# Optimization experiments

Measured on AMD Instinct MI355X. Metric: run time of the kernel, lower is better.

The kernel has to match this reference:

```python
import jax, jax.numpy as jnp
import numpy as np

NBINS = 256

def _rescale_0_1(img):
    return (img + 1.0) * (127.0 / 255.0)

def _rescale_back(img):
    return img * (255.0 / 127.0) - 1.0

def _rgb_to_yuv_y(img):
    # tf.image.rgb_to_yuv luma coefficients; only Y channel is used downstream
    return img[..., 0] * 0.299 + img[..., 1] * 0.587 + img[..., 2] * 0.114

def _equalize_histogram(image):
    # tf.histogram_fixed_width over [0,1] with 256 bins (values clipped to range)
    idx = jnp.clip((image * NBINS).astype(jnp.int32), 0, NBINS - 1)
    hist = jnp.zeros((NBINS,), jnp.int32).at[idx.reshape(-1)].add(1)
    cdf = jnp.cumsum(hist)
    cdf_min = jnp.min(cdf)
    pix_cnt = image.shape[0] * image.shape[1]
    return (cdf - cdf_min).astype(jnp.float32) / jnp.float32(pix_cnt - 1)

def _interpolate(dx, dy, x):
    # brute-force searchsorted substitute: first index where dx - x > 0
    del_vals = dx[jnp.newaxis, :] - x[:, jnp.newaxis]          # [N, 256]
    ind_1 = jnp.argmax(jnp.sign(del_vals), axis=1)             # first positive
    ind_0 = jnp.clip(ind_1 - 1, 0, NBINS - 1)
    dx0, dx1 = dx[ind_0], dx[ind_1]
    dy0, dy1 = dy[ind_0], dy[ind_1]
    denom = dx1 - dx0
    safe_denom = jnp.where(denom == 0, jnp.float32(1.0), denom)
    interp = dy0 + (dy1 - dy0) * (x - dx0) / safe_denom
    return jnp.where(x <= dx[0], dy[0], jnp.where(x >= dx[-1], dy[-1], interp))

def setup_inputs() -> dict:
    key = jax.random.key(0)
    k1, k2 = jax.random.split(key)
    H, W = 1024, 1024
    src = jax.random.uniform(k1, (H, W, 3), jnp.float32, minval=-1.0, maxval=1.0)
    tgt = jax.random.uniform(k2, (H, W, 3), jnp.float32, minval=-1.0, maxval=1.0)
    return {"src": src, "tgt": tgt}

def reference(src, tgt):
    src = _rescale_0_1(src)
    tgt = _rescale_0_1(tgt)
    tgt_y = _rgb_to_yuv_y(tgt)
    h, w = src.shape[0], src.shape[1]
    floating_space = jnp.clip(jnp.arange(0.0, 1.00001, 1.0 / 255.0, dtype=jnp.float32), 0.0, 1.0)
    source = src[:, :, 0]
    cdfsrc = _equalize_histogram(source)
    cdftgt = _equalize_histogram(tgt_y)
    pxmap = _interpolate(cdftgt, floating_space, cdfsrc)
    pxmap = _interpolate(floating_space, pxmap, source.reshape(h * w))
    pxmap = pxmap.reshape(h, w, 1)
    res = jnp.clip(pxmap, 0.0, 1.0)
    return _rescale_back(res)
```

## Files before the change

kernel.cpp:

```cpp
#include <hip/hip_runtime.h>

#define NBINS 256

__device__ __forceinline__ float fs_val(int j) {
    const float c = (float)(1.0 / 255.0);
    float v = (float)j * c;
    return v > 1.0f ? 1.0f : v;
}

__device__ __forceinline__ int bin_of(float s) {
    int i = (int)(s * 256.0f);
    i = i < 0 ? 0 : i;
    i = i > NBINS - 1 ? NBINS - 1 : i;
    return i;
}

__global__ void hm_hist(const float* __restrict__ src,
                        const float* __restrict__ tgt,
                        int* __restrict__ histS, int* __restrict__ histT,
                        int nquad) {
    __shared__ int hs[NBINS];
    __shared__ int ht[NBINS];
    for (int i = threadIdx.x; i < NBINS; i += blockDim.x) { hs[i] = 0; ht[i] = 0; }
    __syncthreads();

    const float c1 = (float)(127.0 / 255.0);
    int tid = blockIdx.x * blockDim.x + threadIdx.x;
    int stride = gridDim.x * blockDim.x;

    for (int q = tid; q < nquad; q += stride) {
        const float4* s4 = (const float4*)(src + 12 * (size_t)q);
        float4 a = s4[0], b = s4[1], c = s4[2];
        float p0 = (a.x + 1.0f) * c1;
        float p1 = (a.w + 1.0f) * c1;
        float p2 = (b.z + 1.0f) * c1;
        float p3 = (c.y + 1.0f) * c1;
        atomicAdd(&hs[bin_of(p0)], 1);
        atomicAdd(&hs[bin_of(p1)], 1);
        atomicAdd(&hs[bin_of(p2)], 1);
        atomicAdd(&hs[bin_of(p3)], 1);

        const float4* t4 = (const float4*)(tgt + 12 * (size_t)q);
        float4 ta = t4[0], tb = t4[1], tc = t4[2];
        {
            float r = (ta.x + 1.0f) * c1, g = (ta.y + 1.0f) * c1, bb = (ta.z + 1.0f) * c1;
            float y = r * 0.299f + g * 0.587f + bb * 0.114f;
            atomicAdd(&ht[bin_of(y)], 1);
        }
        {
            float r = (ta.w + 1.0f) * c1, g = (tb.x + 1.0f) * c1, bb = (tb.y + 1.0f) * c1;
            float y = r * 0.299f + g * 0.587f + bb * 0.114f;
            atomicAdd(&ht[bin_of(y)], 1);
        }
        {
            float r = (tb.z + 1.0f) * c1, g = (tb.w + 1.0f) * c1, bb = (tc.x + 1.0f) * c1;
            float y = r * 0.299f + g * 0.587f + bb * 0.114f;
            atomicAdd(&ht[bin_of(y)], 1);
        }
        {
            float r = (tc.y + 1.0f) * c1, g = (tc.z + 1.0f) * c1, bb = (tc.w + 1.0f) * c1;
            float y = r * 0.299f + g * 0.587f + bb * 0.114f;
            atomicAdd(&ht[bin_of(y)], 1);
        }
    }
    __syncthreads();
    for (int i = threadIdx.x; i < NBINS; i += blockDim.x) {
        if (hs[i]) atomicAdd(&histS[i], hs[i]);
        if (ht[i]) atomicAdd(&histT[i], ht[i]);
    }
}

__global__ void hm_cdf_map(const int* __restrict__ histS,
                           const int* __restrict__ histT,
                           float* __restrict__ pxmap, int npix) {
    __shared__ int sS[NBINS];
    __shared__ int sT[NBINS];
    __shared__ float cdfT[NBINS];
    int t = threadIdx.x;
    sS[t] = histS[t];
    sT[t] = histT[t];
    __syncthreads();
    for (int off = 1; off < NBINS; off <<= 1) {
        int vS = sS[t], vT = sT[t];
        int aS = (t >= off) ? sS[t - off] : 0;
        int aT = (t >= off) ? sT[t - off] : 0;
        __syncthreads();
        sS[t] = vS + aS;
        sT[t] = vT + aT;
        __syncthreads();
    }
    int minS = sS[0], minT = sT[0];
    float denomN = (float)(npix - 1);
    float xS = (float)(sS[t] - minS) / denomN;
    cdfT[t] = (float)(sT[t] - minT) / denomN;
    __syncthreads();

    float res;
    if (xS <= cdfT[0]) {
        res = fs_val(0);
    } else if (xS >= cdfT[NBINS - 1]) {
        res = fs_val(NBINS - 1);
    } else {
        int lo = 0, hi = NBINS - 1;
        while (hi - lo > 1) {
            int mid = (lo + hi) >> 1;
            if (cdfT[mid] > xS) hi = mid; else lo = mid;
        }
        int j1 = hi, j0 = hi - 1;
        float dx0 = cdfT[j0], dx1 = cdfT[j1];
        float dy0 = fs_val(j0), dy1 = fs_val(j1);
        res = dy0 + (dy1 - dy0) * (xS - dx0) / (dx1 - dx0);
    }
    pxmap[t] = res;
}

__global__ void hm_apply(const float* __restrict__ src,
                         const float* __restrict__ pxmap,
                         float* __restrict__ out, int nquad) {
    __shared__ float pm[NBINS];
    for (int i = threadIdx.x; i < NBINS; i += blockDim.x) pm[i] = pxmap[i];
    __syncthreads();

    const float c1 = (float)(127.0 / 255.0);
    const float c2 = (float)(255.0 / 127.0);
    int tid = blockIdx.x * blockDim.x + threadIdx.x;
    int stride = gridDim.x * blockDim.x;

    for (int q = tid; q < nquad; q += stride) {
        const float4* s4 = (const float4*)(src + 12 * (size_t)q);
        float4 a = s4[0], b = s4[1], c = s4[2];
        float xs0 = a.x, xs1 = a.w, xs2 = b.z, xs3 = c.y;
        float4 o;
        float xv[4] = {xs0, xs1, xs2, xs3};
        float ov[4];
        #pragma unroll
        for (int k = 0; k < 4; ++k) {
            float x = (xv[k] + 1.0f) * c1;
            float r;
            if (x <= 0.0f) {
                r = pm[0];
            } else if (x >= 1.0f) {
                r = pm[NBINS - 1];
            } else {
                int g = (int)(x * 255.0f) + 1;
                g = g < 1 ? 1 : (g > NBINS - 1 ? NBINS - 1 : g);
                while (g < NBINS - 1 && fs_val(g) <= x) ++g;
                while (g > 1 && fs_val(g - 1) > x) --g;
                int j1 = g, j0 = g - 1;
                float dx0 = fs_val(j0), dx1 = fs_val(j1);
                r = pm[j0] + (pm[j1] - pm[j0]) * (x - dx0) / (dx1 - dx0);
            }
            r = r < 0.0f ? 0.0f : (r > 1.0f ? 1.0f : r);
            ov[k] = r * c2 - 1.0f;
        }
        o.x = ov[0]; o.y = ov[1]; o.z = ov[2]; o.w = ov[3];
        ((float4*)out)[q] = o;
    }
}

extern "C" void kernel_launch(void* const* d_in, const int* in_sizes, int n_in,
                              void* d_out, int out_size, void* d_ws, size_t ws_size,
                              hipStream_t stream) {
    const float* src = (const float*)d_in[0];
    const float* tgt = (const float*)d_in[1];
    float* out = (float*)d_out;

    int npix = out_size;
    int nquad = npix >> 2;

    int* histS = (int*)d_ws;
    int* histT = histS + NBINS;
    float* pxmap = (float*)(histT + NBINS);

    hipMemsetAsync(d_ws, 0, 2 * NBINS * sizeof(int), stream);

    hm_hist<<<256, 256, 0, stream>>>(src, tgt, histS, histT, nquad);

    hm_cdf_map<<<1, NBINS, 0, stream>>>(histS, histT, pxmap, npix);

    int blocks = (nquad + 255) / 256;
    hm_apply<<<blocks, 256, 0, stream>>>(src, pxmap, out, nquad);
}
```

Measured before the change: 83.35 us.

## Fuse histogram, CDF mapping and apply into one cooperative kernel

Replaces the memset and three kernel launches with a single cooperative kernel of 512 blocks that builds the histograms, grid-syncs, has every block redundantly compute the CDF and pixel map, and then writes the output. Each thread keeps the source values of its first two quads in registers so those pixels are not re-read. This removes launch gaps and the separate memset, at the cost of two grid-wide barriers and redundant per-block scan work. Zeroing the global histogram with atomicExch before the first grid sync depends on the sync ordering to be correct.

```diff
diff --git a/kernel.cpp b/kernel.cpp
--- a/kernel.cpp
+++ b/kernel.cpp
@@ -1,6 +1,9 @@
 #include <hip/hip_runtime.h>
+#include <hip/hip_cooperative_groups.h>
 
 #define NBINS 256
+
+namespace cg = cooperative_groups;
 
 __device__ __forceinline__ float fs_val(int j) {
     const float c = (float)(1.0 / 255.0);
@@ -15,84 +18,122 @@
     return i;
 }
 
-__global__ void hm_hist(const float* __restrict__ src,
-                        const float* __restrict__ tgt,
-                        int* __restrict__ histS, int* __restrict__ histT,
-                        int nquad) {
+__device__ __forceinline__ float4 hist_quad(const float* __restrict__ src,
+                                            const float* __restrict__ tgt,
+                                            int q, int* hs, int* ht) {
+    const float c1 = (float)(127.0 / 255.0);
+    const float4* s4 = (const float4*)(src + 12 * (size_t)q);
+    float4 a = s4[0], b = s4[1], c = s4[2];
+    float p0 = (a.x + 1.0f) * c1;
+    float p1 = (a.w + 1.0f) * c1;
+    float p2 = (b.z + 1.0f) * c1;
+    float p3 = (c.y + 1.0f) * c1;
+    atomicAdd(&hs[bin_of(p0)], 1);
+    atomicAdd(&hs[bin_of(p1)], 1);
+    atomicAdd(&hs[bin_of(p2)], 1);
+    atomicAdd(&hs[bin_of(p3)], 1);
+
+    const float4* t4 = (const float4*)(tgt + 12 * (size_t)q);
+    float4 ta = t4[0], tb = t4[1], tc = t4[2];
+    {
+        float r = (ta.x + 1.0f) * c1, g = (ta.y + 1.0f) * c1, bb = (ta.z + 1.0f) * c1;
+        float y = r * 0.299f + g * 0.587f + bb * 0.114f;
+        atomicAdd(&ht[bin_of(y)], 1);
+    }
+    {
+        float r = (ta.w + 1.0f) * c1, g = (tb.x + 1.0f) * c1, bb = (tb.y + 1.0f) * c1;
+        float y = r * 0.299f + g * 0.587f + bb * 0.114f;
+        atomicAdd(&ht[bin_of(y)], 1);
+    }
+    {
+        float r = (tb.z + 1.0f) * c1, g = (tb.w + 1.0f) * c1, bb = (tc.x + 1.0f) * c1;
+        float y = r * 0.299f + g * 0.587f + bb * 0.114f;
+        atomicAdd(&ht[bin_of(y)], 1);
+    }
+    {
+        float r = (tc.y + 1.0f) * c1, g = (tc.z + 1.0f) * c1, bb = (tc.w + 1.0f) * c1;
+        float y = r * 0.299f + g * 0.587f + bb * 0.114f;
+        atomicAdd(&ht[bin_of(y)], 1);
+    }
+    return make_float4(p0, p1, p2, p3);
+}
+
+__device__ __forceinline__ float map1(float x, const float* pm) {
+    const float c2 = (float)(255.0 / 127.0);
+    float r;
+    if (x <= 0.0f) {
+        r = pm[0];
+    } else if (x >= 1.0f) {
+        r = pm[NBINS - 1];
+    } else {
+        int g = (int)(x * 255.0f) + 1;
+        g = g < 1 ? 1 : (g > NBINS - 1 ? NBINS - 1 : g);
+        while (g < NBINS - 1 && fs_val(g) <= x) ++g;
+        while (g > 1 && fs_val(g - 1) > x) --g;
+        int j1 = g, j0 = g - 1;
+        float dx0 = fs_val(j0), dx1 = fs_val(j1);
+        r = pm[j0] + (pm[j1] - pm[j0]) * (x - dx0) / (dx1 - dx0);
+    }
+    r = r < 0.0f ? 0.0f : (r > 1.0f ? 1.0f : r);
+    return r * c2 - 1.0f;
+}
+
+__global__ void __launch_bounds__(256, 4)
+hm_fused(const float* __restrict__ src, const float* __restrict__ tgt,
+         float* __restrict__ out, int* __restrict__ histS, int* __restrict__ histT,
+         int nquad, int npix) {
     __shared__ int hs[NBINS];
     __shared__ int ht[NBINS];
-    for (int i = threadIdx.x; i < NBINS; i += blockDim.x) { hs[i] = 0; ht[i] = 0; }
+    __shared__ float cdfT[NBINS];
+    __shared__ float pm[NBINS];
+
+    cg::grid_group grid = cg::this_grid();
+
+    const int t = threadIdx.x;
+    const int gid = blockIdx.x * blockDim.x + t;
+    const int nthreads = gridDim.x * blockDim.x;
+
+    hs[t] = 0;
+    ht[t] = 0;
+    if (gid < NBINS)          atomicExch(&histS[gid], 0);
+    else if (gid < 2 * NBINS) atomicExch(&histT[gid - NBINS], 0);
     __syncthreads();
 
-    const float c1 = (float)(127.0 / 255.0);
-    int tid = blockIdx.x * blockDim.x + threadIdx.x;
-    int stride = gridDim.x * blockDim.x;
+    const int q0 = gid;
+    const int q1 = gid + nthreads;
+    float4 xa = make_float4(0.f, 0.f, 0.f, 0.f);
+    float4 xb = make_float4(0.f, 0.f, 0.f, 0.f);
+    if (q0 < nquad) xa = hist_quad(src, tgt, q0, hs, ht);
+    if (q1 < nquad) xb = hist_quad(src, tgt, q1, hs, ht);
+    for (int q = gid + 2 * nthreads; q < nquad; q += nthreads)
+        (void)hist_quad(src, tgt, q, hs, ht);
+    __syncthreads();
 
-    for (int q = tid; q < nquad; q += stride) {
-        const float4* s4 = (const float4*)(src + 12 * (size_t)q);
-        float4 a = s4[0], b = s4[1], c = s4[2];
-        float p0 = (a.x + 1.0f) * c1;
-        float p1 = (a.w + 1.0f) * c1;
-        float p2 = (b.z + 1.0f) * c1;
-        float p3 = (c.y + 1.0f) * c1;
-        atomicAdd(&hs[bin_of(p0)], 1);
-        atomicAdd(&hs[bin_of(p1)], 1);
-        atomicAdd(&hs[bin_of(p2)], 1);
-        atomicAdd(&hs[bin_of(p3)], 1);
+    grid.sync();
 
-        const float4* t4 = (const float4*)(tgt + 12 * (size_t)q);
-        float4 ta = t4[0], tb = t4[1], tc = t4[2];
-        {
-            float r = (ta.x + 1.0f) * c1, g = (ta.y + 1.0f) * c1, bb = (ta.z + 1.0f) * c1;
-            float y = r * 0.299f + g * 0.587f + bb * 0.114f;
-            atomicAdd(&ht[bin_of(y)], 1);
-        }
-        {
-            float r = (ta.w + 1.0f) * c1, g = (tb.x + 1.0f) * c1, bb = (tb.y + 1.0f) * c1;
-            float y = r * 0.299f + g * 0.587f + bb * 0.114f;
-            atomicAdd(&ht[bin_of(y)], 1);
-        }
-        {
-            float r = (tb.z + 1.0f) * c1, g = (tb.w + 1.0f) * c1, bb = (tc.x + 1.0f) * c1;
-            float y = r * 0.299f + g * 0.587f + bb * 0.114f;
-            atomicAdd(&ht[bin_of(y)], 1);
-        }
-        {
-            float r = (tc.y + 1.0f) * c1, g = (tc.z + 1.0f) * c1, bb = (tc.w + 1.0f) * c1;
-            float y = r * 0.299f + g * 0.587f + bb * 0.114f;
-            atomicAdd(&ht[bin_of(y)], 1);
-        }
-    }
-    __syncthreads();
-    for (int i = threadIdx.x; i < NBINS; i += blockDim.x) {
-        if (hs[i]) atomicAdd(&histS[i], hs[i]);
-        if (ht[i]) atomicAdd(&histT[i], ht[i]);
-    }
-}
+    if (hs[t]) atomicAdd(&histS[t], hs[t]);
+    if (ht[t]) atomicAdd(&histT[t], ht[t]);
 
-__global__ void hm_cdf_map(const int* __restrict__ histS,
-                           const int* __restrict__ histT,
-                           float* __restrict__ pxmap, int npix) {
-    __shared__ int sS[NBINS];
-    __shared__ int sT[NBINS];
-    __shared__ float cdfT[NBINS];
-    int t = threadIdx.x;
-    sS[t] = histS[t];
-    sT[t] = histT[t];
+    grid.sync();
+
+    int vS = histS[t];
+    int vT = histT[t];
+    hs[t] = vS;
+    ht[t] = vT;
     __syncthreads();
     for (int off = 1; off < NBINS; off <<= 1) {
-        int vS = sS[t], vT = sT[t];
-        int aS = (t >= off) ? sS[t - off] : 0;
-        int aT = (t >= off) ? sT[t - off] : 0;
+        int cS = hs[t], cT = ht[t];
+        int aS = (t >= off) ? hs[t - off] : 0;
+        int aT = (t >= off) ? ht[t - off] : 0;
         __syncthreads();
-        sS[t] = vS + aS;
-        sT[t] = vT + aT;
+        hs[t] = cS + aS;
+        ht[t] = cT + aT;
         __syncthreads();
     }
-    int minS = sS[0], minT = sT[0];
+    int minS = hs[0], minT = ht[0];
     float denomN = (float)(npix - 1);
-    float xS = (float)(sS[t] - minS) / denomN;
-    cdfT[t] = (float)(sT[t] - minT) / denomN;
+    float xS = (float)(hs[t] - minS) / denomN;
+    cdfT[t] = (float)(ht[t] - minT) / denomN;
     __syncthreads();
 
     float res;
@@ -111,49 +152,25 @@
         float dy0 = fs_val(j0), dy1 = fs_val(j1);
         res = dy0 + (dy1 - dy0) * (xS - dx0) / (dx1 - dx0);
     }
-    pxmap[t] = res;
-}
-
-__global__ void hm_apply(const float* __restrict__ src,
-                         const float* __restrict__ pxmap,
-                         float* __restrict__ out, int nquad) {
-    __shared__ float pm[NBINS];
-    for (int i = threadIdx.x; i < NBINS; i += blockDim.x) pm[i] = pxmap[i];
+    pm[t] = res;
     __syncthreads();
 
+    if (q0 < nquad) {
+        float4 o = make_float4(map1(xa.x, pm), map1(xa.y, pm), map1(xa.z, pm), map1(xa.w, pm));
+        ((float4*)out)[q0] = o;
+    }
+    if (q1 < nquad) {
+        float4 o = make_float4(map1(xb.x, pm), map1(xb.y, pm), map1(xb.z, pm), map1(xb.w, pm));
+        ((float4*)out)[q1] = o;
+    }
     const float c1 = (float)(127.0 / 255.0);
-    const float c2 = (float)(255.0 / 127.0);
-    int tid = blockIdx.x * blockDim.x + threadIdx.x;
-    int stride = gridDim.x * blockDim.x;
-
-    for (int q = tid; q < nquad; q += stride) {
+    for (int q = gid + 2 * nthreads; q < nquad; q += nthreads) {
         const float4* s4 = (const float4*)(src + 12 * (size_t)q);
         float4 a = s4[0], b = s4[1], c = s4[2];
-        float xs0 = a.x, xs1 = a.w, xs2 = b.z, xs3 = c.y;
-        float4 o;
-        float xv[4] = {xs0, xs1, xs2, xs3};
-        float ov[4];
-        #pragma unroll
-        for (int k = 0; k < 4; ++k) {
-            float x = (xv[k] + 1.0f) * c1;
-            float r;
-            if (x <= 0.0f) {
-                r = pm[0];
-            } else if (x >= 1.0f) {
-                r = pm[NBINS - 1];
-            } else {
-                int g = (int)(x * 255.0f) + 1;
-                g = g < 1 ? 1 : (g > NBINS - 1 ? NBINS - 1 : g);
-                while (g < NBINS - 1 && fs_val(g) <= x) ++g;
-                while (g > 1 && fs_val(g - 1) > x) --g;
-                int j1 = g, j0 = g - 1;
-                float dx0 = fs_val(j0), dx1 = fs_val(j1);
-                r = pm[j0] + (pm[j1] - pm[j0]) * (x - dx0) / (dx1 - dx0);
-            }
-            r = r < 0.0f ? 0.0f : (r > 1.0f ? 1.0f : r);
-            ov[k] = r * c2 - 1.0f;
-        }
-        o.x = ov[0]; o.y = ov[1]; o.z = ov[2]; o.w = ov[3];
+        float4 o = make_float4(map1((a.x + 1.0f) * c1, pm),
+                               map1((a.w + 1.0f) * c1, pm),
+                               map1((b.z + 1.0f) * c1, pm),
+                               map1((c.y + 1.0f) * c1, pm));
         ((float4*)out)[q] = o;
     }
 }
@@ -170,14 +187,9 @@
 
     int* histS = (int*)d_ws;
     int* histT = histS + NBINS;
-    float* pxmap = (float*)(histT + NBINS);
 
-    hipMemsetAsync(d_ws, 0, 2 * NBINS * sizeof(int), stream);
-
-    hm_hist<<<256, 256, 0, stream>>>(src, tgt, histS, histT, nquad);
-
-    hm_cdf_map<<<1, NBINS, 0, stream>>>(histS, histT, pxmap, npix);
-
-    int blocks = (nquad + 255) / 256;
-    hm_apply<<<blocks, 256, 0, stream>>>(src, pxmap, out, nquad);
+    dim3 gridDim(512), blockDim(256);
+    void* args[] = { (void*)&src, (void*)&tgt, (void*)&out,
+                     (void*)&histS, (void*)&histT, (void*)&nquad, (void*)&npix };
+    hipLaunchCooperativeKernel((const void*)hm_fused, gridDim, blockDim, args, 0, stream);
 }
```

Result: slower. 193.6 us (+132.3%).
